# Performance work log

Hardware: AMD Instinct MI355X
Metric: run time of the kernel (lower is better)

## Reference

```python
import jax, jax.numpy as jnp
import numpy as np

# Constants from __init__ (domain bounds)
X_MIN, X_MAX = -1.0, 1.0
Y_MIN, Y_MAX = -1.0, 1.0
T_MIN, T_MAX = 0.0, 1.0

N_POINTS = 262144
WIDTH = 128
N_HIDDEN_STACK = 5  # hidden->hidden layers between first and last


def setup_inputs() -> dict:
    key = jax.random.key(0)
    ks = jax.random.split(key, 8)
    X = jax.random.uniform(ks[0], (N_POINTS, 4), dtype=jnp.float32)
    # glorot_normal-ish init
    def glorot(k, fan_in, fan_out, shape):
        std = (2.0 / (fan_in + fan_out)) ** 0.5
        return jax.random.normal(k, shape, dtype=jnp.float32) * std
    W0 = glorot(ks[1], 4, WIDTH, (4, WIDTH))
    b0 = jnp.zeros((WIDTH,), dtype=jnp.float32)
    Wh = glorot(ks[2], WIDTH, WIDTH, (N_HIDDEN_STACK, WIDTH, WIDTH))
    bh = jnp.zeros((N_HIDDEN_STACK, WIDTH), dtype=jnp.float32)
    WL = glorot(ks[3], WIDTH, 2, (WIDTH, 2))
    bL = jnp.zeros((2,), dtype=jnp.float32)
    nu_min = jnp.zeros((), dtype=jnp.float32)
    nu_max = jnp.ones((), dtype=jnp.float32)
    return {"X": X, "nu_min": nu_min, "nu_max": nu_max,
            "W0": W0, "b0": b0, "Wh": Wh, "bh": bh, "WL": WL, "bL": bL}


def _swish(x):
    return x * jax.nn.sigmoid(x)


def reference(X, nu_min, nu_max, W0, b0, Wh, bh, WL, bL):
    # Input rescaling to [-1, 1] per feature, then concat
    x_s = 2.0 * (X[:, 0:1] - X_MIN) / (X_MAX - X_MIN) - 1.0
    y_s = 2.0 * (X[:, 1:2] - Y_MIN) / (Y_MAX - Y_MIN) - 1.0
    t_s = 2.0 * (X[:, 2:3] - T_MIN) / (T_MAX - T_MIN) - 1.0
    nu_s = 2.0 * (X[:, 3:4] - nu_min) / (nu_max - nu_min) - 1.0
    H = jnp.concatenate([x_s, y_s, t_s, nu_s], axis=1)  # [N, 4]
    # Stacked small dense + swish layers (fused-MLP candidate)
    H = _swish(H @ W0 + b0)  # [N, WIDTH]
    for i in range(Wh.shape[0]):
        H = _swish(H @ Wh[i] + bh[i])
    return H @ WL + bL  # [N, 2], no activation on output layer
```

## Files before the change

kernel.cpp:

```cpp
#include <hip/hip_runtime.h>

typedef __bf16 bf16x8 __attribute__((ext_vector_type(8)));
typedef __bf16 bf16x2 __attribute__((ext_vector_type(2)));
typedef float  f32x4  __attribute__((ext_vector_type(4)));

#define WS_WT0_B 0
#define WS_WTH_B 8192
#define WS_WLT_B 172032

__device__ __forceinline__ unsigned short f2b(float f) {
  return __builtin_bit_cast(unsigned short, (__bf16)f);
}

__global__ void prep_kernel(const float* __restrict__ W0,
                            const float* __restrict__ Wh,
                            const float* __restrict__ WL,
                            unsigned short* __restrict__ ws) {
  int i = blockIdx.x * 256 + threadIdx.x;
  int l  = (i >> 3) & 63;
  int j  = i & 7;
  int lm = l & 15, lh = l >> 4;
  if (i < 4096) {
    int nt = i >> 9;
    int n = nt * 16 + lm, k = lh * 8 + j;
    ws[i] = f2b(k < 4 ? W0[k * 128 + n] : 0.f);
  } else if (i < 86016) {
    int t = i - 4096;
    int frag = t >> 9;
    int nt = frag & 7, ks = (frag >> 3) & 3, h = frag >> 5;
    int n = nt * 16 + lm, k = ks * 32 + lh * 8 + j;
    ws[i] = f2b(Wh[(h * 128 + k) * 128 + n]);
  } else if (i < 90112) {
    int t = i - 86016;
    int f = t >> 9;
    int k = (f & 3) * 32 + lh * 8 + j;
    ws[i] = f2b((f < 4 && lm < 2) ? WL[k * 2 + lm] : 0.f);
  }
}

__device__ __forceinline__ f32x4 swish4(f32x4 z) {
  const f32x4 u = z * (-1.44269504088896340736f);
  f32x4 e;
#if __has_builtin(__builtin_amdgcn_exp2f)
  e[0] = __builtin_amdgcn_exp2f(u[0]); e[1] = __builtin_amdgcn_exp2f(u[1]);
  e[2] = __builtin_amdgcn_exp2f(u[2]); e[3] = __builtin_amdgcn_exp2f(u[3]);
#else
  e[0] = __expf(u[0] * 0.6931471805599453f); e[1] = __expf(u[1] * 0.6931471805599453f);
  e[2] = __expf(u[2] * 0.6931471805599453f); e[3] = __expf(u[3] * 0.6931471805599453f);
#endif
  const f32x4 w = e + 1.f;
  f32x4 s;
  s[0] = __builtin_amdgcn_rcpf(w[0]); s[1] = __builtin_amdgcn_rcpf(w[1]);
  s[2] = __builtin_amdgcn_rcpf(w[2]); s[3] = __builtin_amdgcn_rcpf(w[3]);
  return z * s;
}

__device__ __forceinline__ uint2 pack4(f32x4 r) {
  bf16x2 lo = {(__bf16)r[0], (__bf16)r[1]};
  bf16x2 hi = {(__bf16)r[2], (__bf16)r[3]};
  uint2 wv;
  wv.x = __builtin_bit_cast(unsigned int, lo);
  wv.y = __builtin_bit_cast(unsigned int, hi);
  return wv;
}

#define SB() __builtin_amdgcn_sched_barrier(0)
#define GLD(addr) __builtin_bit_cast(bf16x8, *reinterpret_cast<const uint4*>(addr))
#define LRD(addr) __builtin_bit_cast(bf16x8, *reinterpret_cast<const uint4*>(addr))
#define MFMA(a, b, c) __builtin_amdgcn_mfma_f32_16x16x32_bf16((a), (b), (c), 0, 0, 0)

__launch_bounds__(64, 3)
__global__ void mlp_kernel(const float* __restrict__ X,
                           const float* __restrict__ nu_min_p,
                           const float* __restrict__ nu_max_p,
                           const float* __restrict__ b0,
                           const float* __restrict__ bh,
                           const float* __restrict__ bL,
                           const unsigned short* __restrict__ ws,
                           float* __restrict__ out) {
  __shared__ __align__(16) char smem[32 * 256 + 5 * 128 * 4];
  char* Hs = smem;
  float* bias_lds = reinterpret_cast<float*>(smem + 8192);
  const int lane = threadIdx.x;
  const int lm = lane & 15, lh = lane >> 4;
  const int row0 = blockIdx.x * 32;
  const char* ap = reinterpret_cast<const char*>(ws) + lane * 16;
  const int xorm = (lm & 7) << 4;
  const int va0 = lm * 256 + ((lh * 16) ^ xorm);
  const int va1 = va0 + 16 * 256;
  const int wa0 = lm * 256 + ((lh * 8) ^ xorm);
  const int wa1 = wa0 + 16 * 256;

  bf16x8 aL0[8];
#pragma unroll
  for (int nt = 0; nt < 8; ++nt) aL0[nt] = GLD(ap + WS_WT0_B + nt * 1024);
  f32x4 bv0[8];
#pragma unroll
  for (int nt = 0; nt < 8; ++nt)
    bv0[nt] = *reinterpret_cast<const f32x4*>(b0 + nt * 16 + lh * 4);
  float bstg[10];
#pragma unroll
  for (int i = 0; i < 10; ++i) bstg[i] = bh[i * 64 + lane];

  if (lane < 32) {
    const float4 xv = reinterpret_cast<const float4*>(X)[row0 + lane];
    const float numin = nu_min_p[0], numax = nu_max_p[0];
    const float v0 = xv.x;
    const float v1 = xv.y;
    const float v2 = 2.f * xv.z - 1.f;
    const float v3 = 2.f * (xv.w - numin) / (numax - numin) - 1.f;
    uint4 c0;
    c0.x = (unsigned)f2b(v0) | ((unsigned)f2b(v1) << 16);
    c0.y = (unsigned)f2b(v2) | ((unsigned)f2b(v3) << 16);
    c0.z = 0u; c0.w = 0u;
    const uint4 z4 = make_uint4(0u, 0u, 0u, 0u);
    const int xr = (lane & 7) << 4;
    char* rp = Hs + lane * 256;
    *reinterpret_cast<uint4*>(rp + (0  ^ xr)) = c0;
    *reinterpret_cast<uint4*>(rp + (16 ^ xr)) = z4;
    *reinterpret_cast<uint4*>(rp + (32 ^ xr)) = z4;
    *reinterpret_cast<uint4*>(rp + (48 ^ xr)) = z4;
  }
#pragma unroll
  for (int i = 0; i < 10; ++i) bias_lds[i * 64 + lane] = bstg[i];

  f32x4 acc[8][2];
  bf16x8 bfrA[2], bfrB[2];
  bf16x8 aA[8], aB[8];

  bfrA[0] = LRD(Hs + va0);
  bfrA[1] = LRD(Hs + va1);
#pragma unroll
  for (int nt = 0; nt < 8; ++nt) {
    acc[nt][0] = MFMA(aL0[nt], bfrA[0], bv0[nt]);
    acc[nt][1] = MFMA(aL0[nt], bfrA[1], bv0[nt]);
  }
#pragma unroll
  for (int nt = 0; nt < 8; ++nt) aA[nt] = GLD(ap + WS_WTH_B + nt * 1024);
#pragma unroll
  for (int nt = 0; nt < 8; ++nt) {
#pragma unroll
    for (int pt = 0; pt < 2; ++pt) {
      const uint2 wv = pack4(swish4(acc[nt][pt]));
      *reinterpret_cast<uint2*>(Hs + ((pt ? wa1 : wa0) ^ (nt << 5))) = wv;
    }
  }

  const f32x4 zero4 = {0.f, 0.f, 0.f, 0.f};

#pragma unroll 1
  for (int h = 0; h < 5; ++h) {
    const char* wb = ap + WS_WTH_B + h * 32768;
    const float* bl = bias_lds + h * 128;

    bfrA[0] = LRD(Hs + va0);
    bfrA[1] = LRD(Hs + va1);
#pragma unroll
    for (int nt = 0; nt < 8; ++nt) aB[nt] = GLD(wb + 8192 + nt * 1024);
    bfrB[0] = LRD(Hs + (va0 ^ 64));
    bfrB[1] = LRD(Hs + (va1 ^ 64));
#pragma unroll
    for (int nt = 0; nt < 8; ++nt) {
      acc[nt][0] = MFMA(aA[nt], bfrA[0], zero4);
      acc[nt][1] = MFMA(aA[nt], bfrA[1], zero4);
    }
    SB();
#pragma unroll
    for (int nt = 0; nt < 8; ++nt) aA[nt] = GLD(wb + 16384 + nt * 1024);
    bfrA[0] = LRD(Hs + (va0 ^ 128));
    bfrA[1] = LRD(Hs + (va1 ^ 128));
#pragma unroll
    for (int nt = 0; nt < 8; ++nt) {
      acc[nt][0] = MFMA(aB[nt], bfrB[0], acc[nt][0]);
      acc[nt][1] = MFMA(aB[nt], bfrB[1], acc[nt][1]);
    }
    SB();
#pragma unroll
    for (int nt = 0; nt < 8; ++nt) aB[nt] = GLD(wb + 24576 + nt * 1024);
    bfrB[0] = LRD(Hs + (va0 ^ 192));
    bfrB[1] = LRD(Hs + (va1 ^ 192));
#pragma unroll
    for (int nt = 0; nt < 8; ++nt) {
      acc[nt][0] = MFMA(aA[nt], bfrA[0], acc[nt][0]);
      acc[nt][1] = MFMA(aA[nt], bfrA[1], acc[nt][1]);
    }
    SB();
#pragma unroll
    for (int nt = 0; nt < 8; ++nt) aA[nt] = GLD(wb + 32768 + nt * 1024);
#pragma unroll
    for (int nt = 0; nt < 8; ++nt) {
      acc[nt][0] = MFMA(aB[nt], bfrB[0], acc[nt][0]);
      acc[nt][1] = MFMA(aB[nt], bfrB[1], acc[nt][1]);
    }
    SB();
#pragma unroll
    for (int nt = 0; nt < 8; ++nt) {
      const f32x4 bv = *reinterpret_cast<const f32x4*>(bl + nt * 16 + lh * 4);
#pragma unroll
      for (int pt = 0; pt < 2; ++pt) {
        const uint2 wv = pack4(swish4(acc[nt][pt] + bv));
        *reinterpret_cast<uint2*>(Hs + ((pt ? wa1 : wa0) ^ (nt << 5))) = wv;
      }
    }
  }

  {
    const float bl0 = bL[0], bl1 = bL[1];
#pragma unroll
    for (int pt = 0; pt < 2; ++pt) {
      f32x4 accL = {0.f, 0.f, 0.f, 0.f};
#pragma unroll
      for (int ks = 0; ks < 4; ++ks) {
        const bf16x8 bfr = LRD(Hs + ((pt ? va1 : va0) ^ (ks << 6)));
        accL = MFMA(aA[ks], bfr, accL);
      }
      if (lh == 0) {
        const int p = pt * 16 + lm;
        float2 o;
        o.x = accL[0] + bl0;
        o.y = accL[1] + bl1;
        *reinterpret_cast<float2*>(out + (size_t)(row0 + p) * 2) = o;
      }
    }
  }
}

extern "C" void kernel_launch(void* const* d_in, const int* in_sizes, int n_in,
                              void* d_out, int out_size, void* d_ws, size_t ws_size,
                              hipStream_t stream) {
  const float* X     = (const float*)d_in[0];
  const float* numin = (const float*)d_in[1];
  const float* numax = (const float*)d_in[2];
  const float* W0    = (const float*)d_in[3];
  const float* b0    = (const float*)d_in[4];
  const float* bh    = (const float*)d_in[5 + 1];
  const float* Wh    = (const float*)d_in[5];
  const float* WL    = (const float*)d_in[7];
  const float* bL    = (const float*)d_in[8];
  unsigned short* ws = (unsigned short*)d_ws;
  float* out = (float*)d_out;

  hipLaunchKernelGGL(prep_kernel, dim3(352), dim3(256), 0, stream, W0, Wh, WL, ws);
  hipLaunchKernelGGL(mlp_kernel, dim3(8192), dim3(64), 0, stream,
                     X, numin, numax, b0, bh, bL, ws, out);
}
```

Measured before the change: 77.77 us.

## Share weight tiles across four waves via LDS double-buffered staging

Moves from one 64-thread wave per block, where each wave loads every weight fragment from global memory, to 256-thread blocks of four waves. The waves cooperatively stage 8KB weight slices into double-buffered LDS using global_load_lds and read them back as MFMA operands. This cuts global and L2 weight traffic by about four times, at the cost of block-wide barriers between every K-slice phase and extra LDS reads. LDS use per block grows to about 50KB, which may limit how many blocks fit on a CU.

Result: no change. 76.70 us, median of 2 (-1.4%).

```diff
diff --git a/kernel.cpp b/kernel.cpp
--- a/kernel.cpp
+++ b/kernel.cpp
@@ -64,12 +64,27 @@
   return wv;
 }
 
-#define SB() __builtin_amdgcn_sched_barrier(0)
-#define GLD(addr) __builtin_bit_cast(bf16x8, *reinterpret_cast<const uint4*>(addr))
 #define LRD(addr) __builtin_bit_cast(bf16x8, *reinterpret_cast<const uint4*>(addr))
 #define MFMA(a, b, c) __builtin_amdgcn_mfma_f32_16x16x32_bf16((a), (b), (c), 0, 0, 0)
 
-__launch_bounds__(64, 3)
+__device__ __forceinline__ void stage8k(const char* src, char* dst, int tid) {
+  const int woff = (tid >> 6) * 1024;
+#if __has_builtin(__builtin_amdgcn_global_load_lds)
+  __builtin_amdgcn_global_load_lds(
+      (const __attribute__((address_space(1))) unsigned int*)(src + tid * 16),
+      (__attribute__((address_space(3))) unsigned int*)(dst + woff), 16, 0, 0);
+  __builtin_amdgcn_global_load_lds(
+      (const __attribute__((address_space(1))) unsigned int*)(src + 4096 + tid * 16),
+      (__attribute__((address_space(3))) unsigned int*)(dst + 4096 + woff), 16, 0, 0);
+#else
+  const uint4 v0 = *reinterpret_cast<const uint4*>(src + tid * 16);
+  const uint4 v1 = *reinterpret_cast<const uint4*>(src + 4096 + tid * 16);
+  *reinterpret_cast<uint4*>(dst + tid * 16) = v0;
+  *reinterpret_cast<uint4*>(dst + 4096 + tid * 16) = v1;
+#endif
+}
+
+__launch_bounds__(256, 3)
 __global__ void mlp_kernel(const float* __restrict__ X,
                            const float* __restrict__ nu_min_p,
                            const float* __restrict__ nu_max_p,
@@ -78,30 +93,32 @@
                            const float* __restrict__ bL,
                            const unsigned short* __restrict__ ws,
                            float* __restrict__ out) {
-  __shared__ __align__(16) char smem[32 * 256 + 5 * 128 * 4];
-  char* Hs = smem;
-  float* bias_lds = reinterpret_cast<float*>(smem + 8192);
-  const int lane = threadIdx.x;
+  __shared__ __align__(16) char smem[32768 + 16384 + 2560];
+  const int tid  = threadIdx.x;
+  const int lane = tid & 63, wave = tid >> 6;
+  char* Hs  = smem + wave * 8192;
+  char* wb0 = smem + 32768;
+  char* wb1 = smem + 40960;
+  float* bias_lds = reinterpret_cast<float*>(smem + 49152);
   const int lm = lane & 15, lh = lane >> 4;
-  const int row0 = blockIdx.x * 32;
-  const char* ap = reinterpret_cast<const char*>(ws) + lane * 16;
+  const int row0 = blockIdx.x * 128 + wave * 32;
+  const char* wsb = reinterpret_cast<const char*>(ws);
   const int xorm = (lm & 7) << 4;
   const int va0 = lm * 256 + ((lh * 16) ^ xorm);
-  const int va1 = va0 + 16 * 256;
+  const int va1 = va0 + 4096;
   const int wa0 = lm * 256 + ((lh * 8) ^ xorm);
-  const int wa1 = wa0 + 16 * 256;
-
-  bf16x8 aL0[8];
-#pragma unroll
-  for (int nt = 0; nt < 8; ++nt) aL0[nt] = GLD(ap + WS_WT0_B + nt * 1024);
+  const int wa1 = wa0 + 4096;
+
+  stage8k(wsb + WS_WT0_B, wb0, tid);
   f32x4 bv0[8];
 #pragma unroll
   for (int nt = 0; nt < 8; ++nt)
     bv0[nt] = *reinterpret_cast<const f32x4*>(b0 + nt * 16 + lh * 4);
-  float bstg[10];
-#pragma unroll
-  for (int i = 0; i < 10; ++i) bstg[i] = bh[i * 64 + lane];
-
+#pragma unroll
+  for (int i = 0; i < 3; ++i) {
+    const int idx = i * 256 + tid;
+    if (idx < 640) bias_lds[idx] = bh[idx];
+  }
   if (lane < 32) {
     const float4 xv = reinterpret_cast<const float4*>(X)[row0 + lane];
     const float numin = nu_min_p[0], numax = nu_max_p[0];
@@ -121,22 +138,24 @@
     *reinterpret_cast<uint4*>(rp + (32 ^ xr)) = z4;
     *reinterpret_cast<uint4*>(rp + (48 ^ xr)) = z4;
   }
-#pragma unroll
-  for (int i = 0; i < 10; ++i) bias_lds[i * 64 + lane] = bstg[i];
+  __syncthreads();
 
   f32x4 acc[8][2];
-  bf16x8 bfrA[2], bfrB[2];
-  bf16x8 aA[8], aB[8];
-
-  bfrA[0] = LRD(Hs + va0);
-  bfrA[1] = LRD(Hs + va1);
-#pragma unroll
-  for (int nt = 0; nt < 8; ++nt) {
-    acc[nt][0] = MFMA(aL0[nt], bfrA[0], bv0[nt]);
-    acc[nt][1] = MFMA(aL0[nt], bfrA[1], bv0[nt]);
-  }
-#pragma unroll
-  for (int nt = 0; nt < 8; ++nt) aA[nt] = GLD(ap + WS_WTH_B + nt * 1024);
+  bf16x8 aa[8];
+  const f32x4 zero4 = {0.f, 0.f, 0.f, 0.f};
+
+  stage8k(wsb + WS_WTH_B, wb1, tid);
+#pragma unroll
+  for (int nt = 0; nt < 8; ++nt) aa[nt] = LRD(wb0 + nt * 1024 + lane * 16);
+  {
+    const bf16x8 f0 = LRD(Hs + va0);
+    const bf16x8 f1 = LRD(Hs + va1);
+#pragma unroll
+    for (int nt = 0; nt < 8; ++nt) {
+      acc[nt][0] = MFMA(aa[nt], f0, bv0[nt]);
+      acc[nt][1] = MFMA(aa[nt], f1, bv0[nt]);
+    }
+  }
 #pragma unroll
   for (int nt = 0; nt < 8; ++nt) {
 #pragma unroll
@@ -145,54 +164,35 @@
       *reinterpret_cast<uint2*>(Hs + ((pt ? wa1 : wa0) ^ (nt << 5))) = wv;
     }
   }
-
-  const f32x4 zero4 = {0.f, 0.f, 0.f, 0.f};
+  __syncthreads();
+
+#define HPHASE(RBUF, SBUF, SRC, KSOFF, FIRST)                              \
+  do {                                                                     \
+    stage8k((SRC), (SBUF), tid);                                           \
+    _Pragma("unroll")                                                      \
+    for (int nt = 0; nt < 8; ++nt) aa[nt] = LRD((RBUF) + nt * 1024 + lane * 16); \
+    const bf16x8 f0 = LRD(Hs + (va0 ^ (KSOFF)));                           \
+    const bf16x8 f1 = LRD(Hs + (va1 ^ (KSOFF)));                           \
+    _Pragma("unroll")                                                      \
+    for (int nt = 0; nt < 8; ++nt) {                                       \
+      acc[nt][0] = MFMA(aa[nt], f0, (FIRST) ? zero4 : acc[nt][0]);         \
+      acc[nt][1] = MFMA(aa[nt], f1, (FIRST) ? zero4 : acc[nt][1]);         \
+    }                                                                      \
+  } while (0)
 
 #pragma unroll 1
   for (int h = 0; h < 5; ++h) {
-    const char* wb = ap + WS_WTH_B + h * 32768;
+    const char* wsrc = wsb + WS_WTH_B + h * 32768;
     const float* bl = bias_lds + h * 128;
-
-    bfrA[0] = LRD(Hs + va0);
-    bfrA[1] = LRD(Hs + va1);
-#pragma unroll
-    for (int nt = 0; nt < 8; ++nt) aB[nt] = GLD(wb + 8192 + nt * 1024);
-    bfrB[0] = LRD(Hs + (va0 ^ 64));
-    bfrB[1] = LRD(Hs + (va1 ^ 64));
-#pragma unroll
-    for (int nt = 0; nt < 8; ++nt) {
-      acc[nt][0] = MFMA(aA[nt], bfrA[0], zero4);
-      acc[nt][1] = MFMA(aA[nt], bfrA[1], zero4);
-    }
-    SB();
-#pragma unroll
-    for (int nt = 0; nt < 8; ++nt) aA[nt] = GLD(wb + 16384 + nt * 1024);
-    bfrA[0] = LRD(Hs + (va0 ^ 128));
-    bfrA[1] = LRD(Hs + (va1 ^ 128));
-#pragma unroll
-    for (int nt = 0; nt < 8; ++nt) {
-      acc[nt][0] = MFMA(aB[nt], bfrB[0], acc[nt][0]);
-      acc[nt][1] = MFMA(aB[nt], bfrB[1], acc[nt][1]);
-    }
-    SB();
-#pragma unroll
-    for (int nt = 0; nt < 8; ++nt) aB[nt] = GLD(wb + 24576 + nt * 1024);
-    bfrB[0] = LRD(Hs + (va0 ^ 192));
-    bfrB[1] = LRD(Hs + (va1 ^ 192));
-#pragma unroll
-    for (int nt = 0; nt < 8; ++nt) {
-      acc[nt][0] = MFMA(aA[nt], bfrA[0], acc[nt][0]);
-      acc[nt][1] = MFMA(aA[nt], bfrA[1], acc[nt][1]);
-    }
-    SB();
-#pragma unroll
-    for (int nt = 0; nt < 8; ++nt) aA[nt] = GLD(wb + 32768 + nt * 1024);
-#pragma unroll
-    for (int nt = 0; nt < 8; ++nt) {
-      acc[nt][0] = MFMA(aB[nt], bfrB[0], acc[nt][0]);
-      acc[nt][1] = MFMA(aB[nt], bfrB[1], acc[nt][1]);
-    }
-    SB();
+    const char* nsrc = (h < 4) ? (wsrc + 32768) : (wsb + WS_WLT_B);
+
+    HPHASE(wb1, wb0, wsrc + 8192,  0,   true);
+    __syncthreads();
+    HPHASE(wb0, wb1, wsrc + 16384, 64,  false);
+    __syncthreads();
+    HPHASE(wb1, wb0, wsrc + 24576, 128, false);
+    __syncthreads();
+    HPHASE(wb0, wb1, nsrc,         192, false);
 #pragma unroll
     for (int nt = 0; nt < 8; ++nt) {
       const f32x4 bv = *reinterpret_cast<const f32x4*>(bl + nt * 16 + lh * 4);
@@ -202,17 +202,20 @@
         *reinterpret_cast<uint2*>(Hs + ((pt ? wa1 : wa0) ^ (nt << 5))) = wv;
       }
     }
+    __syncthreads();
   }
 
   {
     const float bl0 = bL[0], bl1 = bL[1];
 #pragma unroll
+    for (int ks = 0; ks < 4; ++ks) aa[ks] = LRD(wb1 + ks * 1024 + lane * 16);
+#pragma unroll
     for (int pt = 0; pt < 2; ++pt) {
       f32x4 accL = {0.f, 0.f, 0.f, 0.f};
 #pragma unroll
       for (int ks = 0; ks < 4; ++ks) {
-        const bf16x8 bfr = LRD(Hs + ((pt ? va1 : va0) ^ (ks << 6)));
-        accL = MFMA(aA[ks], bfr, accL);
+        const bf16x8 f = LRD(Hs + ((pt ? va1 : va0) ^ (ks << 6)));
+        accL = MFMA(aa[ks], f, accL);
       }
       if (lh == 0) {
         const int p = pt * 16 + lm;
@@ -223,6 +226,7 @@
       }
     }
   }
+#undef HPHASE
 }
 
 extern "C" void kernel_launch(void* const* d_in, const int* in_sizes, int n_in,
@@ -233,14 +237,14 @@
   const float* numax = (const float*)d_in[2];
   const float* W0    = (const float*)d_in[3];
   const float* b0    = (const float*)d_in[4];
-  const float* bh    = (const float*)d_in[5 + 1];
   const float* Wh    = (const float*)d_in[5];
+  const float* bh    = (const float*)d_in[6];
   const float* WL    = (const float*)d_in[7];
   const float* bL    = (const float*)d_in[8];
   unsigned short* ws = (unsigned short*)d_ws;
   float* out = (float*)d_out;
 
   hipLaunchKernelGGL(prep_kernel, dim3(352), dim3(256), 0, stream, W0, Wh, WL, ws);
-  hipLaunchKernelGGL(mlp_kernel, dim3(8192), dim3(64), 0, stream,
+  hipLaunchKernelGGL(mlp_kernel, dim3(2048), dim3(256), 0, stream,
                      X, numin, numax, b0, bh, bL, ws, out);
 }
```

## Process 64 rows per wavefront to double weight-fragment reuse across MFMAs

Applied to the files above, without the earlier changes.

Each single-wave block now handles 64 points instead of 32, so every weight fragment loaded from global memory feeds four MFMA column tiles instead of two. The goal is to halve global weight traffic per point and halve the grid size. In exchange the accumulator array doubles to 128 floats per lane, launch bounds drop to 2 waves per SIMD, and LDS per block doubles, which reduces occupancy and the latency hiding that comes with it.

Result: no change. 78.52 us (+1.0%).

```diff
diff --git a/kernel.cpp b/kernel.cpp
--- a/kernel.cpp
+++ b/kernel.cpp
@@ -69,7 +69,7 @@
 #define LRD(addr) __builtin_bit_cast(bf16x8, *reinterpret_cast<const uint4*>(addr))
 #define MFMA(a, b, c) __builtin_amdgcn_mfma_f32_16x16x32_bf16((a), (b), (c), 0, 0, 0)
 
-__launch_bounds__(64, 3)
+__launch_bounds__(64, 2)
 __global__ void mlp_kernel(const float* __restrict__ X,
                            const float* __restrict__ nu_min_p,
                            const float* __restrict__ nu_max_p,
@@ -78,22 +78,20 @@
                            const float* __restrict__ bL,
                            const unsigned short* __restrict__ ws,
                            float* __restrict__ out) {
-  __shared__ __align__(16) char smem[32 * 256 + 5 * 128 * 4];
+  __shared__ __align__(16) char smem[64 * 256 + 5 * 128 * 4];
   char* Hs = smem;
-  float* bias_lds = reinterpret_cast<float*>(smem + 8192);
+  float* bias_lds = reinterpret_cast<float*>(smem + 16384);
   const int lane = threadIdx.x;
   const int lm = lane & 15, lh = lane >> 4;
-  const int row0 = blockIdx.x * 32;
+  const int row0 = blockIdx.x * 64;
   const char* ap = reinterpret_cast<const char*>(ws) + lane * 16;
   const int xorm = (lm & 7) << 4;
   const int va0 = lm * 256 + ((lh * 16) ^ xorm);
-  const int va1 = va0 + 16 * 256;
   const int wa0 = lm * 256 + ((lh * 8) ^ xorm);
-  const int wa1 = wa0 + 16 * 256;
-
-  bf16x8 aL0[8];
-#pragma unroll
-  for (int nt = 0; nt < 8; ++nt) aL0[nt] = GLD(ap + WS_WT0_B + nt * 1024);
+
+  bf16x8 aA[8], aB[8];
+#pragma unroll
+  for (int nt = 0; nt < 8; ++nt) aB[nt] = GLD(ap + WS_WT0_B + nt * 1024);
   f32x4 bv0[8];
 #pragma unroll
   for (int nt = 0; nt < 8; ++nt)
@@ -102,7 +100,7 @@
 #pragma unroll
   for (int i = 0; i < 10; ++i) bstg[i] = bh[i * 64 + lane];
 
-  if (lane < 32) {
+  {
     const float4 xv = reinterpret_cast<const float4*>(X)[row0 + lane];
     const float numin = nu_min_p[0], numax = nu_max_p[0];
     const float v0 = xv.x;
@@ -124,27 +122,25 @@
 #pragma unroll
   for (int i = 0; i < 10; ++i) bias_lds[i * 64 + lane] = bstg[i];
 
-  f32x4 acc[8][2];
-  bf16x8 bfrA[2], bfrB[2];
-  bf16x8 aA[8], aB[8];
-
-  bfrA[0] = LRD(Hs + va0);
-  bfrA[1] = LRD(Hs + va1);
-#pragma unroll
-  for (int nt = 0; nt < 8; ++nt) {
-    acc[nt][0] = MFMA(aL0[nt], bfrA[0], bv0[nt]);
-    acc[nt][1] = MFMA(aL0[nt], bfrA[1], bv0[nt]);
-  }
+  f32x4 acc[8][4];
+  bf16x8 bfrA[4], bfrB[4];
+
+#pragma unroll
+  for (int pt = 0; pt < 4; ++pt) bfrA[pt] = LRD(Hs + va0 + pt * 4096);
+#pragma unroll
+  for (int nt = 0; nt < 8; ++nt)
+#pragma unroll
+    for (int pt = 0; pt < 4; ++pt)
+      acc[nt][pt] = MFMA(aB[nt], bfrA[pt], bv0[nt]);
 #pragma unroll
   for (int nt = 0; nt < 8; ++nt) aA[nt] = GLD(ap + WS_WTH_B + nt * 1024);
 #pragma unroll
-  for (int nt = 0; nt < 8; ++nt) {
-#pragma unroll
-    for (int pt = 0; pt < 2; ++pt) {
+  for (int nt = 0; nt < 8; ++nt)
+#pragma unroll
+    for (int pt = 0; pt < 4; ++pt) {
       const uint2 wv = pack4(swish4(acc[nt][pt]));
-      *reinterpret_cast<uint2*>(Hs + ((pt ? wa1 : wa0) ^ (nt << 5))) = wv;
+      *reinterpret_cast<uint2*>(Hs + ((wa0 + pt * 4096) ^ (nt << 5))) = wv;
     }
-  }
 
   const f32x4 zero4 = {0.f, 0.f, 0.f, 0.f};
 
@@ -153,53 +149,53 @@
     const char* wb = ap + WS_WTH_B + h * 32768;
     const float* bl = bias_lds + h * 128;
 
-    bfrA[0] = LRD(Hs + va0);
-    bfrA[1] = LRD(Hs + va1);
+#pragma unroll
+    for (int pt = 0; pt < 4; ++pt) bfrA[pt] = LRD(Hs + va0 + pt * 4096);
 #pragma unroll
     for (int nt = 0; nt < 8; ++nt) aB[nt] = GLD(wb + 8192 + nt * 1024);
-    bfrB[0] = LRD(Hs + (va0 ^ 64));
-    bfrB[1] = LRD(Hs + (va1 ^ 64));
-#pragma unroll
-    for (int nt = 0; nt < 8; ++nt) {
-      acc[nt][0] = MFMA(aA[nt], bfrA[0], zero4);
-      acc[nt][1] = MFMA(aA[nt], bfrA[1], zero4);
-    }
+#pragma unroll
+    for (int pt = 0; pt < 4; ++pt) bfrB[pt] = LRD(Hs + ((va0 + pt * 4096) ^ 64));
+#pragma unroll
+    for (int nt = 0; nt < 8; ++nt)
+#pragma unroll
+      for (int pt = 0; pt < 4; ++pt)
+        acc[nt][pt] = MFMA(aA[nt], bfrA[pt], zero4);
     SB();
 #pragma unroll
     for (int nt = 0; nt < 8; ++nt) aA[nt] = GLD(wb + 16384 + nt * 1024);
-    bfrA[0] = LRD(Hs + (va0 ^ 128));
-    bfrA[1] = LRD(Hs + (va1 ^ 128));
-#pragma unroll
-    for (int nt = 0; nt < 8; ++nt) {
-      acc[nt][0] = MFMA(aB[nt], bfrB[0], acc[nt][0]);
-      acc[nt][1] = MFMA(aB[nt], bfrB[1], acc[nt][1]);
-    }
+#pragma unroll
+    for (int pt = 0; pt < 4; ++pt) bfrA[pt] = LRD(Hs + ((va0 + pt * 4096) ^ 128));
+#pragma unroll
+    for (int nt = 0; nt < 8; ++nt)
+#pragma unroll
+      for (int pt = 0; pt < 4; ++pt)
+        acc[nt][pt] = MFMA(aB[nt], bfrB[pt], acc[nt][pt]);
     SB();
 #pragma unroll
     for (int nt = 0; nt < 8; ++nt) aB[nt] = GLD(wb + 24576 + nt * 1024);
-    bfrB[0] = LRD(Hs + (va0 ^ 192));
-    bfrB[1] = LRD(Hs + (va1 ^ 192));
-#pragma unroll
-    for (int nt = 0; nt < 8; ++nt) {
-      acc[nt][0] = MFMA(aA[nt], bfrA[0], acc[nt][0]);
-      acc[nt][1] = MFMA(aA[nt], bfrA[1], acc[nt][1]);
-    }
+#pragma unroll
+    for (int pt = 0; pt < 4; ++pt) bfrB[pt] = LRD(Hs + ((va0 + pt * 4096) ^ 192));
+#pragma unroll
+    for (int nt = 0; nt < 8; ++nt)
+#pragma unroll
+      for (int pt = 0; pt < 4; ++pt)
+        acc[nt][pt] = MFMA(aA[nt], bfrA[pt], acc[nt][pt]);
     SB();
 #pragma unroll
     for (int nt = 0; nt < 8; ++nt) aA[nt] = GLD(wb + 32768 + nt * 1024);
 #pragma unroll
-    for (int nt = 0; nt < 8; ++nt) {
-      acc[nt][0] = MFMA(aB[nt], bfrB[0], acc[nt][0]);
-      acc[nt][1] = MFMA(aB[nt], bfrB[1], acc[nt][1]);
-    }
+    for (int nt = 0; nt < 8; ++nt)
+#pragma unroll
+      for (int pt = 0; pt < 4; ++pt)
+        acc[nt][pt] = MFMA(aB[nt], bfrB[pt], acc[nt][pt]);
     SB();
 #pragma unroll
     for (int nt = 0; nt < 8; ++nt) {
       const f32x4 bv = *reinterpret_cast<const f32x4*>(bl + nt * 16 + lh * 4);
 #pragma unroll
-      for (int pt = 0; pt < 2; ++pt) {
+      for (int pt = 0; pt < 4; ++pt) {
         const uint2 wv = pack4(swish4(acc[nt][pt] + bv));
-        *reinterpret_cast<uint2*>(Hs + ((pt ? wa1 : wa0) ^ (nt << 5))) = wv;
+        *reinterpret_cast<uint2*>(Hs + ((wa0 + pt * 4096) ^ (nt << 5))) = wv;
       }
     }
   }
@@ -207,11 +203,11 @@
   {
     const float bl0 = bL[0], bl1 = bL[1];
 #pragma unroll
-    for (int pt = 0; pt < 2; ++pt) {
+    for (int pt = 0; pt < 4; ++pt) {
       f32x4 accL = {0.f, 0.f, 0.f, 0.f};
 #pragma unroll
       for (int ks = 0; ks < 4; ++ks) {
-        const bf16x8 bfr = LRD(Hs + ((pt ? va1 : va0) ^ (ks << 6)));
+        const bf16x8 bfr = LRD(Hs + ((va0 + pt * 4096) ^ (ks << 6)));
         accL = MFMA(aA[ks], bfr, accL);
       }
       if (lh == 0) {
@@ -233,14 +229,14 @@
   const float* numax = (const float*)d_in[2];
   const float* W0    = (const float*)d_in[3];
   const float* b0    = (const float*)d_in[4];
-  const float* bh    = (const float*)d_in[5 + 1];
   const float* Wh    = (const float*)d_in[5];
+  const float* bh    = (const float*)d_in[6];
   const float* WL    = (const float*)d_in[7];
   const float* bL    = (const float*)d_in[8];
   unsigned short* ws = (unsigned short*)d_ws;
   float* out = (float*)d_out;
 
   hipLaunchKernelGGL(prep_kernel, dim3(352), dim3(256), 0, stream, W0, Wh, WL, ws);
-  hipLaunchKernelGGL(mlp_kernel, dim3(8192), dim3(64), 0, stream,
+  hipLaunchKernelGGL(mlp_kernel, dim3(4096), dim3(64), 0, stream,
                      X, numin, numax, b0, bh, bL, ws, out);
 }
```
